# Kernel optimization log

Measured on AMD Instinct MI355X. Metric: run time of the kernel, lower is better.

The kernel has to match this reference:

```python
import jax, jax.numpy as jnp
import numpy as np

D_MODEL = 1024
D_FF = 4096
NUM_EXPERTS = 8
TOP_K = 2
AUX_COEF = 0.01
B, T = 4, 2048


def setup_inputs() -> dict:
    key = jax.random.key(0)
    ks = jax.random.split(key, 6)
    scale = 0.02
    x = jax.random.normal(ks[0], (B, T, D_MODEL), dtype=jnp.float32)
    Wr = jax.random.normal(ks[1], (D_MODEL, NUM_EXPERTS), dtype=jnp.float32) * scale
    W1 = jax.random.normal(ks[2], (NUM_EXPERTS, D_MODEL, D_FF), dtype=jnp.float32) * scale
    b1 = jnp.zeros((NUM_EXPERTS, D_FF), dtype=jnp.float32)
    W2 = jax.random.normal(ks[3], (NUM_EXPERTS, D_FF, D_MODEL), dtype=jnp.float32) * scale
    b2 = jnp.zeros((NUM_EXPERTS, D_MODEL), dtype=jnp.float32)
    return {"x": x, "Wr": Wr, "W1": W1, "b1": b1, "W2": W2, "b2": b2}


def reference(x, Wr, W1, b1, W2, b2):
    b, t, d = x.shape
    N = b * t
    xf = x.reshape(N, d)

    # --- router: top-k over softmax probabilities ---
    logits = xf @ Wr                              # (N, E)
    probs = jax.nn.softmax(logits, axis=-1)       # (N, E)
    gates, idx = jax.lax.top_k(probs, TOP_K)      # (N, k), (N, k)
    gates = gates / jnp.sum(gates, axis=-1, keepdims=True)

    # --- aux load-balance loss (Switch Transformer) ---
    one_hot = jax.nn.one_hot(idx, NUM_EXPERTS, dtype=xf.dtype)  # (N, k, E)
    token_mask = jnp.minimum(one_hot.sum(axis=1), 1.0)          # (N, E)
    f = token_mask.mean(axis=0)                                 # (E,)
    P = probs.mean(axis=0)                                      # (E,)
    aux_loss = AUX_COEF * NUM_EXPERTS * jnp.sum(f * P)

    # --- per-token combine weight for each expert (eval: no capacity drop) ---
    cw = jnp.zeros((N, NUM_EXPERTS), dtype=xf.dtype)
    cw = cw.at[jnp.arange(N)[:, None], idx].add(gates)          # (N, E)

    # --- expert FFNs: dense compute per expert, weighted accumulate ---
    out = jnp.zeros_like(xf)
    for e in range(NUM_EXPERTS):
        h = jax.nn.gelu(xf @ W1[e] + b1[e], approximate=False)  # (N, d_ff)
        y = h @ W2[e] + b2[e]                                   # (N, d)
        out = out + cw[:, e:e + 1] * y

    return out.reshape(b, t, d), aux_loss
```

## Files before the change

kernel.cpp:

```cpp
#include <hip/hip_runtime.h>
#include <cstdint>
#include <cstddef>

#define N_TOK 8192
#define DM 1024
#define DFF 4096
#define NE 8
#define PAD 256
#define CAP (N_TOK * 2 + NE * PAD)

typedef __attribute__((ext_vector_type(8))) short bf16x8;
typedef __attribute__((ext_vector_type(8))) unsigned short u16x8;
typedef __attribute__((ext_vector_type(4))) float f32x4;

__device__ __forceinline__ unsigned short f2bf(float f) {
  union { float f; unsigned u; } v; v.f = f;
  unsigned r = v.u + 0x7FFFu + ((v.u >> 16) & 1u);
  return (unsigned short)(r >> 16);
}
__device__ __forceinline__ float bf2f(unsigned short h) {
  union { unsigned u; float f; } v; v.u = ((unsigned)h) << 16;
  return v.f;
}

__device__ __forceinline__ void async16(unsigned short* l, const unsigned short* g) {
  __builtin_amdgcn_global_load_lds(
      (const __attribute__((address_space(1))) unsigned int*)g,
      (__attribute__((address_space(3))) unsigned int*)l, 16, 0, 0);
}

__global__ __launch_bounds__(256) void router_transpose(
    const float* __restrict__ x, const float* __restrict__ Wr,
    const float* __restrict__ W1, const float* __restrict__ W2,
    unsigned short* __restrict__ W1T, unsigned short* __restrict__ W2T,
    unsigned* __restrict__ counts, float* __restrict__ Psum,
    int* __restrict__ tok_e, float* __restrict__ tok_g, int* __restrict__ tok_ls,
    unsigned* __restrict__ done, int* __restrict__ offs, float* __restrict__ aux_out) {
  __shared__ float tile[64][65];
  __shared__ float ps[NE];
  __shared__ unsigned lcnt[NE];
  __shared__ unsigned base[NE];
  const int bid = blockIdx.x;
  const int tid = threadIdx.x;

  if (bid >= 512) {
    const int b = bid - 512;
    const int z = b >> 10;
    const float* I;
    unsigned short* O;
    int R, C;
    if (z < 8) { I = W1 + (size_t)z * DM * DFF; O = W1T + (size_t)z * DM * DFF; R = DM; C = DFF; }
    else       { I = W2 + (size_t)(z - 8) * DM * DFF; O = W2T + (size_t)(z - 8) * DM * DFF; R = DFF; C = DM; }
    const int nbx = C >> 6;
    const int bt = b & 1023;
    const int bx = bt % nbx, by = bt / nbx;
    const int r0 = by * 64, c0 = bx * 64;
    const int q = tid & 15, p = tid >> 4;
#pragma unroll
    for (int i = 0; i < 4; ++i) {
      const int r = i * 16 + p;
      const float4 v = *(const float4*)&I[(size_t)(r0 + r) * C + c0 + q * 4];
      tile[r][q * 4 + 0] = v.x; tile[r][q * 4 + 1] = v.y;
      tile[r][q * 4 + 2] = v.z; tile[r][q * 4 + 3] = v.w;
    }
    __syncthreads();
#pragma unroll
    for (int i = 0; i < 4; ++i) {
      const int cc = i * 16 + p;
      ushort4 h;
      h.x = f2bf(tile[q * 4 + 0][cc]);
      h.y = f2bf(tile[q * 4 + 1][cc]);
      h.z = f2bf(tile[q * 4 + 2][cc]);
      h.w = f2bf(tile[q * 4 + 3][cc]);
      *(ushort4*)&O[(size_t)(c0 + cc) * R + r0 + q * 4] = h;
    }
    return;
  }

  if (tid < NE) { ps[tid] = 0.f; lcnt[tid] = 0u; }
  __syncthreads();
  const int lane = tid & 63, wid = tid >> 6;
  int li0[4], li1[4];
  unsigned lr0[4], lr1[4];
  float lg0[4], lg1[4];
#pragma unroll
  for (int u = 0; u < 4; ++u) {
    const int t = bid * 16 + wid * 4 + u;
    float a[NE];
#pragma unroll
    for (int e = 0; e < NE; ++e) a[e] = 0.f;
#pragma unroll
    for (int i = 0; i < 4; ++i) {
      const int d0 = i * 256 + lane * 4;
      const float4 v = *(const float4*)&x[(size_t)t * DM + d0];
      const float vv[4] = {v.x, v.y, v.z, v.w};
#pragma unroll
      for (int j = 0; j < 4; ++j) {
        const float* wr = &Wr[(size_t)(d0 + j) * NE];
#pragma unroll
        for (int e = 0; e < NE; ++e) a[e] = fmaf(vv[j], wr[e], a[e]);
      }
    }
#pragma unroll
    for (int e = 0; e < NE; ++e)
      for (int s = 32; s > 0; s >>= 1) a[e] += __shfl_xor(a[e], s);
    float mx = a[0];
#pragma unroll
    for (int e = 1; e < NE; ++e) mx = fmaxf(mx, a[e]);
    float p[NE], s = 0.f;
#pragma unroll
    for (int e = 0; e < NE; ++e) { p[e] = expf(a[e] - mx); s += p[e]; }
    float q[NE];
#pragma unroll
    for (int e = 0; e < NE; ++e) q[e] = p[e] / s;
    int i0 = 0; float b0 = q[0];
#pragma unroll
    for (int e = 1; e < NE; ++e) if (q[e] > b0) { b0 = q[e]; i0 = e; }
    int i1 = -1; float b1v = -1.f;
#pragma unroll
    for (int e = 0; e < NE; ++e) if (e != i0 && q[e] > b1v) { b1v = q[e]; i1 = e; }
    const float gs = q[i0] + q[i1];
    li0[u] = i0; li1[u] = i1;
    lg0[u] = q[i0] / gs; lg1[u] = q[i1] / gs;
    if (lane == 0) {
#pragma unroll
      for (int e = 0; e < NE; ++e) atomicAdd(&ps[e], q[e]);
      lr0[u] = atomicAdd(&lcnt[i0], 1u);
      lr1[u] = atomicAdd(&lcnt[i1], 1u);
    }
  }
  __syncthreads();
  if (tid < NE) {
    base[tid] = atomicAdd(&counts[tid], lcnt[tid]);
    atomicAdd(&Psum[tid], ps[tid]);
  }
  __syncthreads();
  if (lane == 0) {
#pragma unroll
    for (int u = 0; u < 4; ++u) {
      const int t = bid * 16 + wid * 4 + u;
      tok_e[2 * t] = li0[u]; tok_e[2 * t + 1] = li1[u];
      tok_g[2 * t] = lg0[u]; tok_g[2 * t + 1] = lg1[u];
      tok_ls[2 * t] = (int)(base[li0[u]] + lr0[u]);
      tok_ls[2 * t + 1] = (int)(base[li1[u]] + lr1[u]);
    }
  }
  __syncthreads();
  if (tid == 0) {
    __threadfence();
    const unsigned d = atomicAdd(done, 1u);
    if (d == 511u) {
      int o = 0; float aux = 0.f;
#pragma unroll
      for (int e = 0; e < NE; ++e) {
        const unsigned c = atomicAdd(&counts[e], 0u);
        const float pe = atomicAdd(&Psum[e], 0.f);
        offs[e] = o;
        o += (int)((c + (PAD - 1u)) / PAD) * PAD;
        aux += ((float)c / (float)N_TOK) * (pe / (float)N_TOK);
      }
      offs[NE] = o;
      aux_out[0] = 0.01f * (float)NE * aux;
    }
  }
}

__global__ __launch_bounds__(256) void gather_kernel(
    const float* __restrict__ x, const int* __restrict__ tok_e,
    const int* __restrict__ tok_ls, const int* __restrict__ offs,
    int* __restrict__ tok_slot, unsigned short* __restrict__ Xg) {
  const int t = blockIdx.x;
  __shared__ int ss[2];
  if (threadIdx.x < 2) {
    const int k = threadIdx.x;
    const int e = tok_e[2 * t + k];
    const int sl = offs[e] + tok_ls[2 * t + k];
    ss[k] = sl;
    tok_slot[2 * t + k] = sl;
  }
  __syncthreads();
  const int i = threadIdx.x;
  const float4 v = ((const float4*)x)[(size_t)t * 256 + i];
  ushort4 h;
  h.x = f2bf(v.x); h.y = f2bf(v.y); h.z = f2bf(v.z); h.w = f2bf(v.w);
  ((ushort4*)Xg)[(size_t)ss[0] * 256 + i] = h;
  ((ushort4*)Xg)[(size_t)ss[1] * 256 + i] = h;
}

template <int BMODE, bool GELU, typename CT>
__global__ __launch_bounds__(512, 4) void gemmk(
    const unsigned short* __restrict__ Ag, const unsigned short* __restrict__ Bt,
    const float* __restrict__ bias, CT* __restrict__ Cout,
    const int* __restrict__ offs, const int K, const int Nn,
    const size_t c_split_stride) {
  constexpr int BM = (BMODE == 0) ? 256 : 128;
  constexpr int BN = (BMODE == 0) ? 128 : 256;
  constexpr int WN = BN / 64;
  constexpr int AREG = BM * 32;
  constexpr int BREG = BN * 32;
  constexpr int SPLIT = (BMODE == 0) ? 1 : 2;

  int tn, gr, ks;
  if (BMODE == 0) {
    tn = (int)blockIdx.x; gr = (int)blockIdx.y; ks = 0;
  } else {
    const int flat = (int)blockIdx.x;
    const int xr = flat & 7;
    const int rest = flat >> 3;
    tn = rest & 3; ks = (rest >> 2) & 1; gr = ((rest >> 3) << 3) + xr;
  }

  const int grow = gr * BM;
  if (grow >= offs[NE]) return;
  int e = 0;
#pragma unroll
  for (int k = 1; k < NE; ++k) if (offs[k] <= grow) e = k;
  const int kext = K / SPLIT;
  const int nt = kext >> 5;

  const unsigned short* A = Ag + (size_t)grow * K + (size_t)ks * kext;
  const unsigned short* B = Bt + ((size_t)e * Nn + (size_t)tn * BN) * K + (size_t)ks * kext;
  const float* bp = (ks == 0) ? bias : nullptr;
  CT* Cw = Cout + (size_t)ks * c_split_stride;

  extern __shared__ unsigned short lds[];
  unsigned short* LA = lds;
  unsigned short* LB = lds + 3 * AREG;

  const int tid = threadIdx.x;
  const int lane = tid & 63;
  const int wid = tid >> 6;
  const int wm = wid / WN;
  const int wn = wid % WN;
  const int arow = lane & 15;
  const int kc = lane >> 4;

  const int sc = ((kc ^ ((arow >> 1) & 3)) << 3);
  const int aBase = (wm * 64 + arow) * 32 + sc;
  const int bBase = (wn * 64 + arow) * 32 + sc;

  const int swzs = (((tid & 3) ^ ((tid >> 3) & 3)) << 3);
  const unsigned short* sA = A + (size_t)(tid >> 2) * K + swzs;
  const unsigned short* sB = B + (size_t)(tid >> 2) * K + swzs;
  const size_t r128 = (size_t)128 * K;
  const size_t dstw = (size_t)wid * 512;

  auto stgA = [&](int db, size_t kt) {
    async16(LA + db * AREG + dstw, sA + kt);
    if constexpr (BMODE == 0) async16(LA + db * AREG + 4096 + dstw, sA + r128 + kt);
  };
  auto stgB = [&](int db, size_t kt) {
    async16(LB + db * BREG + dstw, sB + kt);
    if constexpr (BMODE == 1) async16(LB + db * BREG + 4096 + dstw, sB + r128 + kt);
  };

  f32x4 acc[4][4];
#pragma unroll
  for (int m = 0; m < 4; ++m)
#pragma unroll
    for (int n = 0; n < 4; ++n) acc[m][n] = (f32x4){0.f, 0.f, 0.f, 0.f};

  stgA(0, 0); stgB(0, 0);
  stgA(1, 32); stgB(1, 32);
  asm volatile("s_waitcnt vmcnt(3)" ::: "memory");
  asm volatile("s_barrier" ::: "memory");

  int d0 = 0;
  for (int T = 0; T < nt; ++T) {
    const int d2 = (d0 >= 1) ? d0 - 1 : d0 + 2;
    const size_t kt2 = (size_t)((T + 2 < nt) ? T + 2 : 0) << 5;
    const int la = d0 * AREG, lb = d0 * BREG;

    bf16x8 afr[4], bfr[4];
#pragma unroll
    for (int mf = 0; mf < 4; ++mf) afr[mf] = *(const bf16x8*)&LA[la + aBase + mf * 512];
#pragma unroll
    for (int nf = 0; nf < 4; ++nf) bfr[nf] = *(const bf16x8*)&LB[lb + bBase + nf * 512];

    stgA(d2, kt2);
    stgB(d2, kt2);

    __builtin_amdgcn_s_setprio(1);
#pragma unroll
    for (int m = 0; m < 4; ++m)
#pragma unroll
      for (int n = 0; n < 4; ++n)
        acc[m][n] = __builtin_amdgcn_mfma_f32_16x16x32_bf16(afr[m], bfr[n], acc[m][n], 0, 0, 0);
    __builtin_amdgcn_s_setprio(0);

    asm volatile("s_waitcnt vmcnt(3)" ::: "memory");
    asm volatile("s_barrier" ::: "memory");
    d0 = (d0 == 2) ? 0 : d0 + 1;
  }
  asm volatile("s_waitcnt vmcnt(0)" ::: "memory");

  const int rl = (lane >> 4) * 4;
  const int cl = lane & 15;
  float bv[4];
#pragma unroll
  for (int n = 0; n < 4; ++n) {
    const int col = tn * BN + wn * 64 + n * 16 + cl;
    bv[n] = bp ? bp[(size_t)e * Nn + col] : 0.f;
  }
#pragma unroll
  for (int m = 0; m < 4; ++m) {
    const int row = grow + wm * 64 + m * 16 + rl;
#pragma unroll
    for (int jj = 0; jj < 4; ++jj) {
      CT* rowp = Cw + (size_t)(row + jj) * Nn + tn * BN + wn * 64 + cl;
#pragma unroll
      for (int n = 0; n < 4; ++n) {
        float v = acc[m][n][jj] + bv[n];
        if (GELU) {
          const float w = -1.5957691216057308f * (v + 0.044715f * v * v * v);
          v = v / (1.f + __expf(w));
        }
        if constexpr (sizeof(CT) == 2) { rowp[n * 16] = (CT)f2bf(v); } else { rowp[n * 16] = (CT)v; }
      }
    }
  }
}

__global__ __launch_bounds__(128) void combine_kernel(
    const unsigned short* __restrict__ Ya, const unsigned short* __restrict__ Yb,
    const int* __restrict__ tok_slot, const float* __restrict__ tok_g,
    float* __restrict__ out) {
  const int t = blockIdx.x;
  const int i = threadIdx.x;
  const int s0 = tok_slot[2 * t], s1 = tok_slot[2 * t + 1];
  const float g0 = tok_g[2 * t], g1 = tok_g[2 * t + 1];
  const u16x8 a0 = ((const u16x8*)Ya)[(size_t)s0 * 128 + i];
  const u16x8 b0 = ((const u16x8*)Yb)[(size_t)s0 * 128 + i];
  const u16x8 a1 = ((const u16x8*)Ya)[(size_t)s1 * 128 + i];
  const u16x8 b1 = ((const u16x8*)Yb)[(size_t)s1 * 128 + i];
  float r[8];
#pragma unroll
  for (int j = 0; j < 8; ++j)
    r[j] = g0 * (bf2f(a0[j]) + bf2f(b0[j])) + g1 * (bf2f(a1[j]) + bf2f(b1[j]));
  float4* op = (float4*)&out[(size_t)t * DM + i * 8];
  op[0] = (float4){r[0], r[1], r[2], r[3]};
  op[1] = (float4){r[4], r[5], r[6], r[7]};
}

extern "C" void kernel_launch(void* const* d_in, const int* in_sizes, int n_in,
                              void* d_out, int out_size, void* d_ws, size_t ws_size,
                              hipStream_t stream) {
  const float* x = (const float*)d_in[0];
  const float* Wr = (const float*)d_in[1];
  const float* W1 = (const float*)d_in[2];
  const float* b1 = (const float*)d_in[3];
  const float* W2 = (const float*)d_in[4];
  const float* b2 = (const float*)d_in[5];
  float* out = (float*)d_out;

  char* w = (char*)d_ws;
  size_t ob = 0;
  auto take = [&](size_t nbytes) -> void* {
    void* p = w + ob;
    ob = (ob + nbytes + 255) & ~(size_t)255;
    return p;
  };
  unsigned short* W2T = (unsigned short*)take((size_t)NE * DM * DFF * 2);
  unsigned short* H = (unsigned short*)take((size_t)CAP * DFF * 2);
  char* R = (char*)take((size_t)NE * DFF * DM * 2 + (size_t)CAP * DM * 2);
  unsigned short* W1T = (unsigned short*)R;
  unsigned short* Xg = (unsigned short*)(R + (size_t)NE * DFF * DM * 2);
  unsigned short* Ya = (unsigned short*)R;
  unsigned short* Yb = (unsigned short*)(R + (size_t)CAP * DM * 2);
  char* cz = (char*)take(128);
  unsigned* counts = (unsigned*)cz;
  float* Psum = (float*)(cz + 32);
  unsigned* done = (unsigned*)(cz + 64);
  int* offs = (int*)take(16 * 4);
  int* tok_e = (int*)take(2 * N_TOK * 4);
  float* tok_g = (float*)take(2 * N_TOK * 4);
  int* tok_ls = (int*)take(2 * N_TOK * 4);
  int* tok_slot = (int*)take(2 * N_TOK * 4);
  (void)ws_size; (void)in_sizes; (void)n_in; (void)out_size;

  hipFuncSetAttribute(reinterpret_cast<const void*>(&gemmk<0, true, unsigned short>),
                      hipFuncAttributeMaxDynamicSharedMemorySize, 73728);
  hipFuncSetAttribute(reinterpret_cast<const void*>(&gemmk<1, false, unsigned short>),
                      hipFuncAttributeMaxDynamicSharedMemorySize, 73728);

  hipMemsetAsync(cz, 0, 128, stream);
  router_transpose<<<512 + 16 * 1024, 256, 0, stream>>>(
      x, Wr, W1, W2, W1T, W2T, counts, Psum, tok_e, tok_g, tok_ls,
      done, offs, out + (size_t)N_TOK * DM);
  gather_kernel<<<N_TOK, 256, 0, stream>>>(x, tok_e, tok_ls, offs, tok_slot, Xg);
  gemmk<0, true, unsigned short><<<dim3(32, CAP / 256), 512, 73728, stream>>>(
      Xg, W1T, b1, H, offs, DM, DFF, 0);
  gemmk<1, false, unsigned short><<<dim3((CAP / 128) * 8), 512, 73728, stream>>>(
      H, W2T, b2, Ya, offs, DFF, DM, (size_t)CAP * DM);
  combine_kernel<<<N_TOK, 128, 0, stream>>>(Ya, Yb, tok_slot, tok_g, out);
}
```

Baseline: 529.3 us.

## Move W2 transpose-convert into the first expert GEMM launch to overlap

The fp32-to-bf16 transpose of W2 moves out of the router kernel and into the first GEMM launch as extra trailing blocks, using 512 threads per block and the GEMM's dynamic LDS as the staging tile. The goal is to overlap the memory-bound W2 conversion with the compute-bound first GEMM and shorten the router kernel. Because the GEMM grid is now flattened and the transpose blocks come last, they may only run in the GEMM's tail. The extra blocks also compete for occupancy.

```diff
diff --git a/kernel.cpp b/kernel.cpp
--- a/kernel.cpp
+++ b/kernel.cpp
@@ -8,6 +8,7 @@
 #define NE 8
 #define PAD 256
 #define CAP (N_TOK * 2 + NE * PAD)
+#define NT1 ((DFF / 128) * (CAP / 256))
 
 typedef __attribute__((ext_vector_type(8))) short bf16x8;
 typedef __attribute__((ext_vector_type(8))) unsigned short u16x8;
@@ -29,10 +30,9 @@
       (__attribute__((address_space(3))) unsigned int*)l, 16, 0, 0);
 }
 
-__global__ __launch_bounds__(256) void router_transpose(
+__global__ __launch_bounds__(256) void router_w1t(
     const float* __restrict__ x, const float* __restrict__ Wr,
-    const float* __restrict__ W1, const float* __restrict__ W2,
-    unsigned short* __restrict__ W1T, unsigned short* __restrict__ W2T,
+    const float* __restrict__ W1, unsigned short* __restrict__ W1T,
     unsigned* __restrict__ counts, float* __restrict__ Psum,
     int* __restrict__ tok_e, float* __restrict__ tok_g, int* __restrict__ tok_ls,
     unsigned* __restrict__ done, int* __restrict__ offs, float* __restrict__ aux_out) {
@@ -46,20 +46,16 @@
   if (bid >= 512) {
     const int b = bid - 512;
     const int z = b >> 10;
-    const float* I;
-    unsigned short* O;
-    int R, C;
-    if (z < 8) { I = W1 + (size_t)z * DM * DFF; O = W1T + (size_t)z * DM * DFF; R = DM; C = DFF; }
-    else       { I = W2 + (size_t)(z - 8) * DM * DFF; O = W2T + (size_t)(z - 8) * DM * DFF; R = DFF; C = DM; }
-    const int nbx = C >> 6;
+    const float* I = W1 + (size_t)z * DM * DFF;
+    unsigned short* O = W1T + (size_t)z * DM * DFF;
     const int bt = b & 1023;
-    const int bx = bt % nbx, by = bt / nbx;
+    const int bx = bt & 63, by = bt >> 6;
     const int r0 = by * 64, c0 = bx * 64;
     const int q = tid & 15, p = tid >> 4;
 #pragma unroll
     for (int i = 0; i < 4; ++i) {
       const int r = i * 16 + p;
-      const float4 v = *(const float4*)&I[(size_t)(r0 + r) * C + c0 + q * 4];
+      const float4 v = *(const float4*)&I[(size_t)(r0 + r) * DFF + c0 + q * 4];
       tile[r][q * 4 + 0] = v.x; tile[r][q * 4 + 1] = v.y;
       tile[r][q * 4 + 2] = v.z; tile[r][q * 4 + 3] = v.w;
     }
@@ -72,7 +68,7 @@
       h.y = f2bf(tile[q * 4 + 1][cc]);
       h.z = f2bf(tile[q * 4 + 2][cc]);
       h.w = f2bf(tile[q * 4 + 3][cc]);
-      *(ushort4*)&O[(size_t)(c0 + cc) * R + r0 + q * 4] = h;
+      *(ushort4*)&O[(size_t)(c0 + cc) * DM + r0 + q * 4] = h;
     }
     return;
   }
@@ -192,7 +188,8 @@
     const unsigned short* __restrict__ Ag, const unsigned short* __restrict__ Bt,
     const float* __restrict__ bias, CT* __restrict__ Cout,
     const int* __restrict__ offs, const int K, const int Nn,
-    const size_t c_split_stride) {
+    const size_t c_split_stride,
+    const float* __restrict__ TW_in, unsigned short* __restrict__ TW_out) {
   constexpr int BM = (BMODE == 0) ? 256 : 128;
   constexpr int BN = (BMODE == 0) ? 128 : 256;
   constexpr int WN = BN / 64;
@@ -200,9 +197,43 @@
   constexpr int BREG = BN * 32;
   constexpr int SPLIT = (BMODE == 0) ? 1 : 2;
 
+  extern __shared__ unsigned short lds[];
+  const int tid = threadIdx.x;
+
   int tn, gr, ks;
   if (BMODE == 0) {
-    tn = (int)blockIdx.x; gr = (int)blockIdx.y; ks = 0;
+    const int flat = (int)blockIdx.x;
+    if (flat >= NT1) {
+      float* tile = (float*)lds;
+      const int b = flat - NT1;
+      const int z = b >> 10;
+      const float* I = TW_in + (size_t)z * DM * DFF;
+      unsigned short* O = TW_out + (size_t)z * DM * DFF;
+      const int bt = b & 1023;
+      const int bx = bt & 15, by = bt >> 4;
+      const int r0 = by * 64, c0 = bx * 64;
+      const int q = tid & 15, p = tid >> 4;
+#pragma unroll
+      for (int i = 0; i < 2; ++i) {
+        const int r = i * 32 + p;
+        const float4 v = *(const float4*)&I[(size_t)(r0 + r) * DM + c0 + q * 4];
+        tile[r * 65 + q * 4 + 0] = v.x; tile[r * 65 + q * 4 + 1] = v.y;
+        tile[r * 65 + q * 4 + 2] = v.z; tile[r * 65 + q * 4 + 3] = v.w;
+      }
+      __syncthreads();
+#pragma unroll
+      for (int i = 0; i < 2; ++i) {
+        const int cc = i * 32 + p;
+        ushort4 h;
+        h.x = f2bf(tile[(q * 4 + 0) * 65 + cc]);
+        h.y = f2bf(tile[(q * 4 + 1) * 65 + cc]);
+        h.z = f2bf(tile[(q * 4 + 2) * 65 + cc]);
+        h.w = f2bf(tile[(q * 4 + 3) * 65 + cc]);
+        *(ushort4*)&O[(size_t)(c0 + cc) * DFF + r0 + q * 4] = h;
+      }
+      return;
+    }
+    tn = flat & 31; gr = flat >> 5; ks = 0;
   } else {
     const int flat = (int)blockIdx.x;
     const int xr = flat & 7;
@@ -223,11 +254,9 @@
   const float* bp = (ks == 0) ? bias : nullptr;
   CT* Cw = Cout + (size_t)ks * c_split_stride;
 
-  extern __shared__ unsigned short lds[];
   unsigned short* LA = lds;
   unsigned short* LB = lds + 3 * AREG;
 
-  const int tid = threadIdx.x;
   const int lane = tid & 63;
   const int wid = tid >> 6;
   const int wm = wid / WN;
@@ -384,13 +413,13 @@
                       hipFuncAttributeMaxDynamicSharedMemorySize, 73728);
 
   hipMemsetAsync(cz, 0, 128, stream);
-  router_transpose<<<512 + 16 * 1024, 256, 0, stream>>>(
-      x, Wr, W1, W2, W1T, W2T, counts, Psum, tok_e, tok_g, tok_ls,
+  router_w1t<<<512 + 8 * 1024, 256, 0, stream>>>(
+      x, Wr, W1, W1T, counts, Psum, tok_e, tok_g, tok_ls,
       done, offs, out + (size_t)N_TOK * DM);
   gather_kernel<<<N_TOK, 256, 0, stream>>>(x, tok_e, tok_ls, offs, tok_slot, Xg);
-  gemmk<0, true, unsigned short><<<dim3(32, CAP / 256), 512, 73728, stream>>>(
-      Xg, W1T, b1, H, offs, DM, DFF, 0);
+  gemmk<0, true, unsigned short><<<dim3(NT1 + 8 * 1024), 512, 73728, stream>>>(
+      Xg, W1T, b1, H, offs, DM, DFF, 0, W2, W2T);
   gemmk<1, false, unsigned short><<<dim3((CAP / 128) * 8), 512, 73728, stream>>>(
-      H, W2T, b2, Ya, offs, DFF, DM, (size_t)CAP * DM);
+      H, W2T, b2, Ya, offs, DFF, DM, (size_t)CAP * DM, nullptr, nullptr);
   combine_kernel<<<N_TOK, 128, 0, stream>>>(Ya, Yb, tok_slot, tok_g, out);
 }
```

Measured after the change: 509.6 us (median of 2 runs). 3.7% less time.
